# Kernel optimization log

Measured on AMD Instinct MI355X. Metric: run time of the kernel, lower is better.

Reference implementation:

```python
import jax, jax.numpy as jnp
import numpy as np

B, N, M, D, H = 4, 2048, 2048, 1024, 16
HD = D // H


def setup_inputs() -> dict:
    key = jax.random.key(0)
    ks = jax.random.split(key, 16)
    s = 1.0 / np.sqrt(D)
    inp = {
        "Q": jax.random.normal(ks[0], (B, N, D), jnp.float32),
        "K": jax.random.normal(ks[1], (B, M, D), jnp.float32),
        "V": jax.random.normal(ks[2], (B, M, D), jnp.float32),
        "attn_bias": jax.random.normal(ks[3], (B, N, M), jnp.float32),
        "mask": jax.random.randint(ks[4], (B, M), 0, 2).astype(bool),
        # linear params (torch nn.Linear: y = x @ W.T + b)
        "Wq": jax.random.uniform(ks[5], (D, D), jnp.float32, -s, s),
        "bq": jax.random.uniform(ks[6], (D,), jnp.float32, -s, s),
        "Wk": jax.random.uniform(ks[7], (D, D), jnp.float32, -s, s),
        "bk": jax.random.uniform(ks[8], (D,), jnp.float32, -s, s),
        "Wv": jax.random.uniform(ks[9], (D, D), jnp.float32, -s, s),
        "bv": jax.random.uniform(ks[10], (D,), jnp.float32, -s, s),
        "Wo": jax.random.uniform(ks[11], (D, D), jnp.float32, -s, s),
        "bo": jax.random.uniform(ks[12], (D,), jnp.float32, -s, s),
    }
    return inp


def reference(Q, K, V, attn_bias, mask, Wq, bq, Wk, bk, Wv, bv, Wo, bo):
    b, n, d = Q.shape
    m = K.shape[1]
    # bias (B,N,M) -> (B,1,N,M); mask (B,M) True = masked out (-inf)
    bias = attn_bias[:, None, :, :]
    bias = jnp.where(mask[:, None, None, :], -jnp.inf, bias)
    # projections, split heads: (B, H, len, head_dim)
    q = (Q @ Wq.T + bq).reshape(b, n, H, HD).transpose(0, 2, 1, 3)
    k = (K @ Wk.T + bk).reshape(b, m, H, HD).transpose(0, 2, 1, 3)
    v = (V @ Wv.T + bv).reshape(b, m, H, HD).transpose(0, 2, 1, 3)
    scale = 1.0 / np.sqrt(HD).astype(np.float32)
    attn = jnp.einsum("bhid,bhjd->bhij", q * scale, k) + bias
    attn = jax.nn.softmax(attn, axis=-1)
    out = jnp.einsum("bhij,bhjd->bhid", attn, v)
    out = out.transpose(0, 2, 1, 3).reshape(b, n, d)
    return out @ Wo.T + bo
```

## Files before the change

### kernel.cpp

```cpp
#include <hip/hip_runtime.h>
#include <hip/hip_bf16.h>

#define Bq 4
#define Nq 2048
#define Mq 2048
#define Dq 1024
#define Hq 16

typedef __attribute__((ext_vector_type(8))) short short8;
typedef __attribute__((ext_vector_type(4))) short short4v;
typedef __attribute__((ext_vector_type(4))) float floatx4;
typedef __attribute__((ext_vector_type(16))) float floatx16;
typedef __attribute__((ext_vector_type(4))) unsigned uint4v;

static __device__ __forceinline__ short f2bf(float f) {
    __hip_bfloat16 h = __float2bfloat16(f);
    short r;
    __builtin_memcpy(&r, &h, 2);
    return r;
}
static __device__ __forceinline__ float bf2f(short s) {
    unsigned u = ((unsigned)(unsigned short)s) << 16;
    float f;
    __builtin_memcpy(&f, &u, 4);
    return f;
}
static __device__ __forceinline__ unsigned cvtpk_bf16(float lo, float hi) {
    unsigned r;
    asm("v_cvt_pk_bf16_f32 %0, %1, %2" : "=v"(r) : "v"(lo), "v"(hi));
    return r;
}
static __device__ __forceinline__ void swap32(unsigned &a, unsigned &b) {
    asm("v_permlane32_swap_b32 %0, %1" : "+v"(a), "+v"(b));
}
static __device__ __forceinline__ float exp2_fast(float x) {
    float r;
    asm("v_exp_f32 %0, %1" : "=v"(r) : "v"(x));
    return r;
}
static __device__ __forceinline__ void gld16(const void* g, void* l) {
    __builtin_amdgcn_global_load_lds(
        (const __attribute__((address_space(1))) unsigned int*)g,
        (__attribute__((address_space(3))) unsigned int*)l, 16, 0, 0);
}

__global__ void bias_prep(const float* __restrict__ bias, const int* __restrict__ mask,
                          short* __restrict__ out)
{
    const long i = ((long)blockIdx.x * 256 + threadIdx.x) * 8;
    const int m = (int)(i & (Mq - 1));
    const int b = (int)(i >> 22);
    floatx4 f0 = *(const floatx4*)(bias + i);
    floatx4 f1 = *(const floatx4*)(bias + i + 4);
    const int* mp = mask + b * Mq + m;
    short8 o;
#pragma unroll
    for (int e = 0; e < 4; ++e) {
        o[e]     = mp[e]     ? f2bf(-1e38f) : f2bf(f0[e] * 1.44269504f);
        o[e + 4] = mp[e + 4] ? f2bf(-1e38f) : f2bf(f1[e] * 1.44269504f);
    }
    *(short8*)(out + i) = o;
}

__global__ void cvt_bf(const float* __restrict__ s0, const float* __restrict__ s1,
                       const float* __restrict__ s2, const float* __restrict__ s3,
                       short* __restrict__ out, long per)
{
    const int z = blockIdx.y;
    const float* s = (z == 0) ? s0 : (z == 1) ? s1 : (z == 2) ? s2 : s3;
    short* d = out + (long)z * per;
    const long i = ((long)blockIdx.x * 256 + threadIdx.x) * 8;
    floatx4 f0 = *(const floatx4*)(s + i);
    floatx4 f1 = *(const floatx4*)(s + i + 4);
    short8 o;
#pragma unroll
    for (int e = 0; e < 4; ++e) { o[e] = f2bf(f0[e]); o[e + 4] = f2bf(f1[e]); }
    *(short8*)(d + i) = o;
}

struct GB {
    const short* A[3];
    const short* W[3];
    const float* bias[3];
    void* C[3];
    float scale[3];
    int omode[3];
};

__global__ __launch_bounds__(256, 3)
void gemm_all(GB gb, int K)
{
    __shared__ __align__(16) short As[2][128 * 32];
    __shared__ __align__(16) short Bs[2][128 * 32];

    const int z = blockIdx.z;
    const short* Ap = gb.A[z];
    const short* Wp = gb.W[z];

    const int tid = threadIdx.x;
    const int lane = tid & 63;
    const int wid = tid >> 6;
    const int wr = wid >> 1, wc = wid & 1;
    const int g = lane >> 4, c = lane & 15;
    const long row0 = (long)blockIdx.x * 128;
    const int col0 = blockIdx.y * 128;

    const int R0 = tid >> 2;
    const int ub = (tid & 3) ^ ((R0 >> 1) & 3);
    const short* asrc = Ap + (row0 + R0) * (long)K + ub * 8;
    const short* bsrc = Wp + ((long)col0 + R0) * K + ub * 8;

    floatx4 acc[4][4];
#pragma unroll
    for (int i = 0; i < 4; ++i)
#pragma unroll
        for (int j = 0; j < 4; ++j) acc[i][j] = (floatx4)0.0f;

#define GSTAGE(buf, koff) do {                                                \
        char* ad = (char*)As + (buf) * 8192 + wid * 1024;                     \
        char* bd = (char*)Bs + (buf) * 8192 + wid * 1024;                     \
        gld16(asrc + (koff), ad);                                             \
        gld16(asrc + 64L * K + (koff), ad + 4096);                            \
        gld16(bsrc + (koff), bd);                                             \
        gld16(bsrc + 64L * K + (koff), bd + 4096);                            \
    } while (0)

    GSTAGE(0, 0);
    __syncthreads();

    int buf = 0;
    for (int kt = 0; kt < K; kt += 32) {
        if (kt + 32 < K) GSTAGE(buf ^ 1, kt + 32);
        short8* As8 = (short8*)((char*)As + buf * 8192);
        short8* Bs8 = (short8*)((char*)Bs + buf * 8192);
        short8 af[4], bfq[4];
#pragma unroll
        for (int fm = 0; fm < 4; ++fm) {
            const int r = wr * 64 + fm * 16 + c;
            af[fm] = As8[r * 4 + (g ^ ((r >> 1) & 3))];
        }
#pragma unroll
        for (int fn = 0; fn < 4; ++fn) {
            const int cc = wc * 64 + fn * 16 + c;
            bfq[fn] = Bs8[cc * 4 + (g ^ ((cc >> 1) & 3))];
        }
#pragma unroll
        for (int fm = 0; fm < 4; ++fm)
#pragma unroll
            for (int fn = 0; fn < 4; ++fn)
                acc[fm][fn] = __builtin_amdgcn_mfma_f32_16x16x32_bf16(af[fm], bfq[fn], acc[fm][fn], 0, 0, 0);
        __syncthreads();
        buf ^= 1;
    }
#undef GSTAGE

    const float sc = gb.scale[z];
    const float* bp = gb.bias[z];
    const int om = gb.omode[z];
    void* Cp = gb.C[z];
#pragma unroll
    for (int fn = 0; fn < 4; ++fn) {
        const int ccol = col0 + wc * 64 + fn * 16 + c;
        const float bv = bp[ccol];
#pragma unroll
        for (int fm = 0; fm < 4; ++fm) {
            const long r0 = row0 + wr * 64 + fm * 16 + g * 4;
#pragma unroll
            for (int reg = 0; reg < 4; ++reg) {
                const float val = (acc[fm][fn][reg] + bv) * sc;
                const long rr = r0 + reg;
                if (om == 0) {
                    ((short*)Cp)[rr * Dq + ccol] = f2bf(val);
                } else if (om == 1) {
                    const long idx = ((long)(rr >> 11) * Dq + ccol) * (long)Mq + (rr & (Mq - 1));
                    ((short*)Cp)[idx] = f2bf(val);
                } else {
                    ((float*)Cp)[rr * Dq + ccol] = val;
                }
            }
        }
    }
}

__global__ __launch_bounds__(256, 4)
void attn_fused(const short* __restrict__ qg_, const short* __restrict__ kg_,
                const short* __restrict__ vtg, const short* __restrict__ bmg,
                short* __restrict__ outg)
{
    __shared__ __align__(16) short k_lds[2][64 * 64];
    __shared__ __align__(16) short v_lds[2][64 * 64];

    const int tid = threadIdx.x;
    const int lane = tid & 63;
    const int w = tid >> 6;
    const int hi = lane >> 5;
    const int q31 = lane & 31;

    const int blk = blockIdx.x;
    const int bh = blk & 63;
    const int qt = blk >> 6;
    const int b = bh >> 4, h = bh & 15;

    const long qbase = (long)b * Nq + qt * 128 + w * 32;

    short8 qf[4];
#pragma unroll
    for (int ks = 0; ks < 4; ++ks)
        qf[ks] = *(const short8*)(qg_ + (qbase + q31) * Dq + h * 64 + ks * 16 + hi * 8);

    floatx16 oa[2];
    oa[0] = (floatx16)0.0f; oa[1] = (floatx16)0.0f;
    float m_s = -1e37f, l_s = 0.0f;

    const int sr = tid >> 3;
    const int su = (tid & 7) ^ (sr & 7);
    const char* ksrc = (const char*)(kg_ + ((long)b * Mq + sr) * Dq + h * 64 + su * 8);
    const char* vsrc = (const char*)(vtg + ((long)b * Dq + h * 64 + sr) * Mq + su * 8);

#define STAGE(bf, kt2) do {                                                   \
        const long j0b = (long)(kt2) * 64;                                    \
        char* kd = (char*)k_lds + (bf) * 8192 + w * 1024;                     \
        char* vd = (char*)v_lds + (bf) * 8192 + w * 1024;                     \
        gld16(ksrc + j0b * (Dq * 2), kd);                                     \
        gld16(ksrc + (j0b + 32) * (Dq * 2), kd + 4096);                       \
        gld16(vsrc + j0b * 2, vd);                                            \
        gld16(vsrc + 32L * Mq * 2 + j0b * 2, vd + 4096);                      \
    } while (0)

    STAGE(0, 0);
    __syncthreads();

    int buf = 0;
    for (int kt = 0; kt < 32; ++kt) {
        if (kt < 31) STAGE(buf ^ 1, kt + 1);
        const short* brow = bmg + (qbase + q31) * Mq + (long)kt * 64;
        short4v bb[8];
#pragma unroll
        for (int kg = 0; kg < 2; ++kg)
#pragma unroll
            for (int Qh = 0; Qh < 4; ++Qh)
                bb[kg * 4 + Qh] = *(const short4v*)(brow + kg * 32 + Qh * 8 + hi * 4);

        const char* kb = (const char*)k_lds + buf * 8192;
        const char* vb = (const char*)v_lds + buf * 8192;

        floatx16 sa[2];
#pragma unroll
        for (int kg = 0; kg < 2; ++kg)
#pragma unroll
            for (int Qh = 0; Qh < 4; ++Qh) {
                const short4v b4 = bb[kg * 4 + Qh];
#pragma unroll
                for (int e = 0; e < 4; ++e)
                    sa[kg][Qh * 4 + e] = bf2f(b4[e]);
            }
#pragma unroll
        for (int kg = 0; kg < 2; ++kg) {
            short8 kf[4];
#pragma unroll
            for (int ks = 0; ks < 4; ++ks) {
                const int r = kg * 32 + q31;
                const int up = (2 * ks + hi) ^ (r & 7);
                kf[ks] = *(const short8*)(kb + r * 128 + up * 16);
            }
#pragma unroll
            for (int ks = 0; ks < 4; ++ks)
                sa[kg] = __builtin_amdgcn_mfma_f32_32x32x16_bf16(kf[ks], qf[ks], sa[kg], 0, 0, 0);
        }

        float p[32];
#pragma unroll
        for (int kg = 0; kg < 2; ++kg)
#pragma unroll
            for (int j = 0; j < 16; ++j)
                p[kg * 16 + j] = sa[kg][j];
        float t16[16];
#pragma unroll
        for (int i = 0; i < 16; ++i) t16[i] = fmaxf(p[2 * i], p[2 * i + 1]);
#pragma unroll
        for (int i = 0; i < 8; ++i) t16[i] = fmaxf(t16[2 * i], t16[2 * i + 1]);
        t16[0] = fmaxf(fmaxf(fmaxf(t16[0], t16[1]), fmaxf(t16[2], t16[3])),
                       fmaxf(fmaxf(t16[4], t16[5]), fmaxf(t16[6], t16[7])));
        const float pm = fmaxf(t16[0], __shfl_xor(t16[0], 32));
        if (!__all(pm <= m_s + 11.5f)) {
            const float mn = fmaxf(m_s, pm);
            const float al = exp2_fast(m_s - mn);
            l_s *= al;
            oa[0] *= al; oa[1] *= al;
            m_s = mn;
        }
#pragma unroll
        for (int i = 0; i < 32; ++i) p[i] = exp2_fast(p[i] - m_s);
        float s16[16];
#pragma unroll
        for (int i = 0; i < 16; ++i) s16[i] = p[2 * i] + p[2 * i + 1];
#pragma unroll
        for (int i = 0; i < 8; ++i) s16[i] = s16[2 * i] + s16[2 * i + 1];
        float rs = ((s16[0] + s16[1]) + (s16[2] + s16[3])) +
                   ((s16[4] + s16[5]) + (s16[6] + s16[7]));
        rs += __shfl_xor(rs, 32);
        l_s += rs;

        uint4v pw[4];
#pragma unroll
        for (int kg = 0; kg < 2; ++kg) {
            unsigned w0 = cvtpk_bf16(p[kg * 16 + 0], p[kg * 16 + 1]);
            unsigned w1 = cvtpk_bf16(p[kg * 16 + 2], p[kg * 16 + 3]);
            unsigned w2 = cvtpk_bf16(p[kg * 16 + 4], p[kg * 16 + 5]);
            unsigned w3 = cvtpk_bf16(p[kg * 16 + 6], p[kg * 16 + 7]);
            swap32(w0, w2); swap32(w1, w3);
            pw[kg * 2][0] = w0; pw[kg * 2][1] = w1; pw[kg * 2][2] = w2; pw[kg * 2][3] = w3;
            unsigned w4 = cvtpk_bf16(p[kg * 16 + 8],  p[kg * 16 + 9]);
            unsigned w5 = cvtpk_bf16(p[kg * 16 + 10], p[kg * 16 + 11]);
            unsigned w6 = cvtpk_bf16(p[kg * 16 + 12], p[kg * 16 + 13]);
            unsigned w7 = cvtpk_bf16(p[kg * 16 + 14], p[kg * 16 + 15]);
            swap32(w4, w6); swap32(w5, w7);
            pw[kg * 2 + 1][0] = w4; pw[kg * 2 + 1][1] = w5; pw[kg * 2 + 1][2] = w6; pw[kg * 2 + 1][3] = w7;
        }

#pragma unroll
        for (int dg = 0; dg < 2; ++dg) {
            short8 vf[4];
#pragma unroll
            for (int ks = 0; ks < 4; ++ks) {
                const int r = dg * 32 + q31;
                const int up = (2 * ks + hi) ^ (r & 7);
                vf[ks] = *(const short8*)(vb + r * 128 + up * 16);
            }
#pragma unroll
            for (int ks = 0; ks < 4; ++ks)
                oa[dg] = __builtin_amdgcn_mfma_f32_32x32x16_bf16(
                    vf[ks], __builtin_bit_cast(short8, pw[ks]), oa[dg], 0, 0, 0);
        }
        __syncthreads();
        buf ^= 1;
    }
#undef STAGE

    const float invl = 1.0f / l_s;
    short* op = outg + (qbase + q31) * Dq + h * 64;
#pragma unroll
    for (int dg = 0; dg < 2; ++dg)
#pragma unroll
        for (int Qh = 0; Qh < 4; ++Qh) {
            short4v t;
#pragma unroll
            for (int e = 0; e < 4; ++e)
                t[e] = f2bf(oa[dg][Qh * 4 + e] * invl);
            *(short4v*)(op + dg * 32 + Qh * 8 + hi * 4) = t;
        }
}

extern "C" void kernel_launch(void* const* d_in, const int* in_sizes, int n_in,
                              void* d_out, int out_size, void* d_ws, size_t ws_size,
                              hipStream_t stream)
{
    const float* Q    = (const float*)d_in[0];
    const float* K    = (const float*)d_in[1];
    const float* V    = (const float*)d_in[2];
    const float* bias = (const float*)d_in[3];
    const int*   mask = (const int*)d_in[4];
    const float* Wq   = (const float*)d_in[5];
    const float* bq   = (const float*)d_in[6];
    const float* Wk   = (const float*)d_in[7];
    const float* bk   = (const float*)d_in[8];
    const float* Wv   = (const float*)d_in[9];
    const float* bv   = (const float*)d_in[10];
    const float* Wo   = (const float*)d_in[11];
    const float* bo   = (const float*)d_in[12];

    const size_t TSZ = (size_t)Bq * Nq * Dq;
    short* q_ws  = (short*)d_ws;
    short* k_ws  = q_ws  + TSZ;
    short* vt_ws = k_ws  + TSZ;
    short* a_ws  = vt_ws + TSZ;
    short* bm_ws = a_ws  + TSZ;
    short* w_ws  = bm_ws + 2 * TSZ;
    short* qin_ws = a_ws;
    short* kin_ws = bm_ws;
    short* vin_ws = bm_ws + TSZ;
    (void)ws_size;

    cvt_bf<<<dim3(512, 4), dim3(256), 0, stream>>>(Wq, Wk, Wv, Wo, w_ws, (long)Dq * Dq);
    cvt_bf<<<dim3(4096, 3), dim3(256), 0, stream>>>(Q, K, V, V, qin_ws, (long)TSZ);

    GB g1{};
    g1.A[0] = qin_ws; g1.A[1] = kin_ws; g1.A[2] = vin_ws;
    g1.W[0] = w_ws; g1.W[1] = w_ws + Dq * Dq; g1.W[2] = w_ws + 2 * Dq * Dq;
    g1.bias[0] = bq; g1.bias[1] = bk; g1.bias[2] = bv;
    g1.C[0] = q_ws; g1.C[1] = k_ws; g1.C[2] = vt_ws;
    g1.scale[0] = 0.125f * 1.44269504f; g1.scale[1] = 1.0f; g1.scale[2] = 1.0f;
    g1.omode[0] = 0; g1.omode[1] = 0; g1.omode[2] = 1;
    gemm_all<<<dim3(64, 8, 3), dim3(256), 0, stream>>>(g1, Dq);

    bias_prep<<<dim3(8192), dim3(256), 0, stream>>>(bias, mask, bm_ws);

    attn_fused<<<dim3(1024), dim3(256), 0, stream>>>(q_ws, k_ws, vt_ws, bm_ws, a_ws);

    GB g2{};
    g2.A[0] = a_ws;
    g2.W[0] = w_ws + 3 * Dq * Dq;
    g2.bias[0] = bo;
    g2.C[0] = d_out;
    g2.scale[0] = 1.0f;
    g2.omode[0] = 2;
    gemm_all<<<dim3(64, 8, 1), dim3(256), 0, stream>>>(g2, Dq);
}
```

Measured before the change: 328.3 us.

## Unroll attention loop by two with prefetched bias registers and MFMA priority

Restructures the flash-attention main loop into a two-step unrolled body with fixed LDS buffer pointers. The bias tile for the next key block is prefetched into a second register set, so global bias loads overlap the current block's compute instead of sitting on its critical path. MFMA sections are wrapped in s_setprio to raise wave priority during matrix work, and accumulators are split into scalar vectors to help register allocation. The second bias register set raises VGPR pressure, which could lower occupancy.

```diff
diff --git a/kernel.cpp b/kernel.cpp
--- a/kernel.cpp
+++ b/kernel.cpp
@@ -208,14 +208,14 @@
     for (int ks = 0; ks < 4; ++ks)
         qf[ks] = *(const short8*)(qg_ + (qbase + q31) * Dq + h * 64 + ks * 16 + hi * 8);
 
-    floatx16 oa[2];
-    oa[0] = (floatx16)0.0f; oa[1] = (floatx16)0.0f;
+    floatx16 oa0 = (floatx16)0.0f, oa1 = (floatx16)0.0f;
     float m_s = -1e37f, l_s = 0.0f;
 
     const int sr = tid >> 3;
     const int su = (tid & 7) ^ (sr & 7);
     const char* ksrc = (const char*)(kg_ + ((long)b * Mq + sr) * Dq + h * 64 + su * 8);
     const char* vsrc = (const char*)(vtg + ((long)b * Dq + h * 64 + sr) * Mq + su * 8);
+    const short* bbase = bmg + (qbase + q31) * Mq + hi * 4;
 
 #define STAGE(bf, kt2) do {                                                   \
         const long j0b = (long)(kt2) * 64;                                    \
@@ -227,128 +227,180 @@
         gld16(vsrc + 32L * Mq * 2 + j0b * 2, vd + 4096);                      \
     } while (0)
 
+#define LOADBB(bb, kt2) do {                                                  \
+        const short* brow_ = bbase + (long)(kt2) * 64;                        \
+        _Pragma("unroll")                                                     \
+        for (int kg = 0; kg < 2; ++kg)                                        \
+            _Pragma("unroll")                                                 \
+            for (int Qh = 0; Qh < 4; ++Qh)                                    \
+                bb[kg * 4 + Qh] = *(const short4v*)(brow_ + kg * 32 + Qh * 8);\
+    } while (0)
+
+#define COMPUTE(kb, vb, bb) do {                                              \
+        floatx16 sa0, sa1;                                                    \
+        _Pragma("unroll")                                                     \
+        for (int Qh = 0; Qh < 4; ++Qh)                                        \
+            _Pragma("unroll")                                                 \
+            for (int e = 0; e < 4; ++e) {                                     \
+                sa0[Qh * 4 + e] = bf2f(bb[Qh][e]);                            \
+                sa1[Qh * 4 + e] = bf2f(bb[4 + Qh][e]);                        \
+            }                                                                 \
+        {                                                                     \
+            short8 kf[4];                                                     \
+            _Pragma("unroll")                                                 \
+            for (int ks = 0; ks < 4; ++ks)                                    \
+                kf[ks] = *(const short8*)((kb) + q31 * 128 + (((2 * ks + hi) ^ (q31 & 7)) * 16)); \
+            __builtin_amdgcn_s_setprio(1);                                    \
+            _Pragma("unroll")                                                 \
+            for (int ks = 0; ks < 4; ++ks)                                    \
+                sa0 = __builtin_amdgcn_mfma_f32_32x32x16_bf16(kf[ks], qf[ks], sa0, 0, 0, 0); \
+            __builtin_amdgcn_s_setprio(0);                                    \
+        }                                                                     \
+        {                                                                     \
+            short8 kf[4];                                                     \
+            const int r1 = 32 + q31;                                          \
+            _Pragma("unroll")                                                 \
+            for (int ks = 0; ks < 4; ++ks)                                    \
+                kf[ks] = *(const short8*)((kb) + r1 * 128 + (((2 * ks + hi) ^ (r1 & 7)) * 16)); \
+            __builtin_amdgcn_s_setprio(1);                                    \
+            _Pragma("unroll")                                                 \
+            for (int ks = 0; ks < 4; ++ks)                                    \
+                sa1 = __builtin_amdgcn_mfma_f32_32x32x16_bf16(kf[ks], qf[ks], sa1, 0, 0, 0); \
+            __builtin_amdgcn_s_setprio(0);                                    \
+        }                                                                     \
+                                 \
+        {                                                                     \
+            float a0 = fmaxf(fmaxf(sa0[0], sa0[1]), fmaxf(sa0[2], sa0[3]));   \
+            float a1 = fmaxf(fmaxf(sa0[4], sa0[5]), fmaxf(sa0[6], sa0[7]));   \
+            float a2 = fmaxf(fmaxf(sa0[8], sa0[9]), fmaxf(sa0[10], sa0[11])); \
+            float a3 = fmaxf(fmaxf(sa0[12], sa0[13]), fmaxf(sa0[14], sa0[15]));\
+            float a4 = fmaxf(fmaxf(sa1[0], sa1[1]), fmaxf(sa1[2], sa1[3]));   \
+            float a5 = fmaxf(fmaxf(sa1[4], sa1[5]), fmaxf(sa1[6], sa1[7]));   \
+            float a6 = fmaxf(fmaxf(sa1[8], sa1[9]), fmaxf(sa1[10], sa1[11])); \
+            float a7 = fmaxf(fmaxf(sa1[12], sa1[13]), fmaxf(sa1[14], sa1[15]));\
+            float pm = fmaxf(fmaxf(fmaxf(a0, a1), fmaxf(a2, a3)),             \
+                             fmaxf(fmaxf(a4, a5), fmaxf(a6, a7)));            \
+            pm = fmaxf(pm, __shfl_xor(pm, 32));                               \
+            if (!__all(pm <= m_s + 11.5f)) {                                  \
+                const float mn = fmaxf(m_s, pm);                              \
+                const float al = exp2_fast(m_s - mn);                         \
+                l_s *= al;                                                    \
+                oa0 *= al; oa1 *= al;                                         \
+                m_s = mn;                                                     \
+            }                                                                 \
+        }                                                                     \
+        _Pragma("unroll")                                                     \
+        for (int j = 0; j < 16; ++j) {                                        \
+            sa0[j] = exp2_fast(sa0[j] - m_s);                                 \
+            sa1[j] = exp2_fast(sa1[j] - m_s);                                 \
+        }                                                                     \
+        {                                                                     \
+            const float t0 = (sa0[0] + sa0[1]) + (sa0[2] + sa0[3]);           \
+            const float t1 = (sa0[4] + sa0[5]) + (sa0[6] + sa0[7]);           \
+            const float t2 = (sa0[8] + sa0[9]) + (sa0[10] + sa0[11]);         \
+            const float t3 = (sa0[12] + sa0[13]) + (sa0[14] + sa0[15]);       \
+            const float t4 = (sa1[0] + sa1[1]) + (sa1[2] + sa1[3]);           \
+            const float t5 = (sa1[4] + sa1[5]) + (sa1[6] + sa1[7]);           \
+            const float t6 = (sa1[8] + sa1[9]) + (sa1[10] + sa1[11]);         \
+            const float t7 = (sa1[12] + sa1[13]) + (sa1[14] + sa1[15]);       \
+            float rs = ((t0 + t1) + (t2 + t3)) + ((t4 + t5) + (t6 + t7));     \
+            rs += __shfl_xor(rs, 32);                                         \
+            l_s += rs;                                                        \
+        }                                                                     \
+        uint4v pw0, pw1, pw2, pw3;                                            \
+        {                                                                     \
+            unsigned w0 = cvtpk_bf16(sa0[0], sa0[1]);                         \
+            unsigned w1 = cvtpk_bf16(sa0[2], sa0[3]);                         \
+            unsigned w2 = cvtpk_bf16(sa0[4], sa0[5]);                         \
+            unsigned w3 = cvtpk_bf16(sa0[6], sa0[7]);                         \
+            swap32(w0, w2); swap32(w1, w3);                                   \
+            pw0[0] = w0; pw0[1] = w1; pw0[2] = w2; pw0[3] = w3;               \
+            unsigned w4 = cvtpk_bf16(sa0[8], sa0[9]);                         \
+            unsigned w5 = cvtpk_bf16(sa0[10], sa0[11]);                       \
+            unsigned w6 = cvtpk_bf16(sa0[12], sa0[13]);                       \
+            unsigned w7 = cvtpk_bf16(sa0[14], sa0[15]);                       \
+            swap32(w4, w6); swap32(w5, w7);                                   \
+            pw1[0] = w4; pw1[1] = w5; pw1[2] = w6; pw1[3] = w7;               \
+            unsigned x0 = cvtpk_bf16(sa1[0], sa1[1]);                         \
+            unsigned x1 = cvtpk_bf16(sa1[2], sa1[3]);                         \
+            unsigned x2 = cvtpk_bf16(sa1[4], sa1[5]);                         \
+            unsigned x3 = cvtpk_bf16(sa1[6], sa1[7]);                         \
+            swap32(x0, x2); swap32(x1, x3);                                   \
+            pw2[0] = x0; pw2[1] = x1; pw2[2] = x2; pw2[3] = x3;               \
+            unsigned x4 = cvtpk_bf16(sa1[8], sa1[9]);                         \
+            unsigned x5 = cvtpk_bf16(sa1[10], sa1[11]);                       \
+            unsigned x6 = cvtpk_bf16(sa1[12], sa1[13]);                       \
+            unsigned x7 = cvtpk_bf16(sa1[14], sa1[15]);                       \
+            swap32(x4, x6); swap32(x5, x7);                                   \
+            pw3[0] = x4; pw3[1] = x5; pw3[2] = x6; pw3[3] = x7;               \
+        }                                                                     \
+        {                                                                     \
+            short8 vf[4];                                                     \
+            _Pragma("unroll")                                                 \
+            for (int ks = 0; ks < 4; ++ks)                                    \
+                vf[ks] = *(const short8*)((vb) + q31 * 128 + (((2 * ks + hi) ^ (q31 & 7)) * 16)); \
+            __builtin_amdgcn_s_setprio(1);                                    \
+            oa0 = __builtin_amdgcn_mfma_f32_32x32x16_bf16(vf[0], __builtin_bit_cast(short8, pw0), oa0, 0, 0, 0); \
+            oa0 = __builtin_amdgcn_mfma_f32_32x32x16_bf16(vf[1], __builtin_bit_cast(short8, pw1), oa0, 0, 0, 0); \
+            oa0 = __builtin_amdgcn_mfma_f32_32x32x16_bf16(vf[2], __builtin_bit_cast(short8, pw2), oa0, 0, 0, 0); \
+            oa0 = __builtin_amdgcn_mfma_f32_32x32x16_bf16(vf[3], __builtin_bit_cast(short8, pw3), oa0, 0, 0, 0); \
+            __builtin_amdgcn_s_setprio(0);                                    \
+        }                                                                     \
+        {                                                                     \
+            short8 vf[4];                                                     \
+            const int r1 = 32 + q31;                                          \
+            _Pragma("unroll")                                                 \
+            for (int ks = 0; ks < 4; ++ks)                                    \
+                vf[ks] = *(const short8*)((vb) + r1 * 128 + (((2 * ks + hi) ^ (r1 & 7)) * 16)); \
+            __builtin_amdgcn_s_setprio(1);                                    \
+            oa1 = __builtin_amdgcn_mfma_f32_32x32x16_bf16(vf[0], __builtin_bit_cast(short8, pw0), oa1, 0, 0, 0); \
+            oa1 = __builtin_amdgcn_mfma_f32_32x32x16_bf16(vf[1], __builtin_bit_cast(short8, pw1), oa1, 0, 0, 0); \
+            oa1 = __builtin_amdgcn_mfma_f32_32x32x16_bf16(vf[2], __builtin_bit_cast(short8, pw2), oa1, 0, 0, 0); \
+            oa1 = __builtin_amdgcn_mfma_f32_32x32x16_bf16(vf[3], __builtin_bit_cast(short8, pw3), oa1, 0, 0, 0); \
+            __builtin_amdgcn_s_setprio(0);                                    \
+        }                                                                     \
+    } while (0)
+
+    short4v bbA[8], bbB[8];
+    const char* kb0 = (const char*)k_lds;
+    const char* kb1 = (const char*)k_lds + 8192;
+    const char* vb0 = (const char*)v_lds;
+    const char* vb1 = (const char*)v_lds + 8192;
+
     STAGE(0, 0);
+    LOADBB(bbA, 0);
     __syncthreads();
 
-    int buf = 0;
-    for (int kt = 0; kt < 32; ++kt) {
-        if (kt < 31) STAGE(buf ^ 1, kt + 1);
-        const short* brow = bmg + (qbase + q31) * Mq + (long)kt * 64;
-        short4v bb[8];
-#pragma unroll
-        for (int kg = 0; kg < 2; ++kg)
-#pragma unroll
-            for (int Qh = 0; Qh < 4; ++Qh)
-                bb[kg * 4 + Qh] = *(const short4v*)(brow + kg * 32 + Qh * 8 + hi * 4);
-
-        const char* kb = (const char*)k_lds + buf * 8192;
-        const char* vb = (const char*)v_lds + buf * 8192;
-
-        floatx16 sa[2];
-#pragma unroll
-        for (int kg = 0; kg < 2; ++kg)
-#pragma unroll
-            for (int Qh = 0; Qh < 4; ++Qh) {
-                const short4v b4 = bb[kg * 4 + Qh];
-#pragma unroll
-                for (int e = 0; e < 4; ++e)
-                    sa[kg][Qh * 4 + e] = bf2f(b4[e]);
-            }
-#pragma unroll
-        for (int kg = 0; kg < 2; ++kg) {
-            short8 kf[4];
-#pragma unroll
-            for (int ks = 0; ks < 4; ++ks) {
-                const int r = kg * 32 + q31;
-                const int up = (2 * ks + hi) ^ (r & 7);
-                kf[ks] = *(const short8*)(kb + r * 128 + up * 16);
-            }
-#pragma unroll
-            for (int ks = 0; ks < 4; ++ks)
-                sa[kg] = __builtin_amdgcn_mfma_f32_32x32x16_bf16(kf[ks], qf[ks], sa[kg], 0, 0, 0);
+    for (int it = 0; it < 16; ++it) {
+        const int t0 = 2 * it;
+        STAGE(1, t0 + 1);
+        LOADBB(bbB, t0 + 1);
+        COMPUTE(kb0, vb0, bbA);
+        __syncthreads();
+        if (it < 15) {
+            STAGE(0, t0 + 2);
+            LOADBB(bbA, t0 + 2);
         }
-
-        float p[32];
-#pragma unroll
-        for (int kg = 0; kg < 2; ++kg)
-#pragma unroll
-            for (int j = 0; j < 16; ++j)
-                p[kg * 16 + j] = sa[kg][j];
-        float t16[16];
-#pragma unroll
-        for (int i = 0; i < 16; ++i) t16[i] = fmaxf(p[2 * i], p[2 * i + 1]);
-#pragma unroll
-        for (int i = 0; i < 8; ++i) t16[i] = fmaxf(t16[2 * i], t16[2 * i + 1]);
-        t16[0] = fmaxf(fmaxf(fmaxf(t16[0], t16[1]), fmaxf(t16[2], t16[3])),
-                       fmaxf(fmaxf(t16[4], t16[5]), fmaxf(t16[6], t16[7])));
-        const float pm = fmaxf(t16[0], __shfl_xor(t16[0], 32));
-        if (!__all(pm <= m_s + 11.5f)) {
-            const float mn = fmaxf(m_s, pm);
-            const float al = exp2_fast(m_s - mn);
-            l_s *= al;
-            oa[0] *= al; oa[1] *= al;
-            m_s = mn;
-        }
-#pragma unroll
-        for (int i = 0; i < 32; ++i) p[i] = exp2_fast(p[i] - m_s);
-        float s16[16];
-#pragma unroll
-        for (int i = 0; i < 16; ++i) s16[i] = p[2 * i] + p[2 * i + 1];
-#pragma unroll
-        for (int i = 0; i < 8; ++i) s16[i] = s16[2 * i] + s16[2 * i + 1];
-        float rs = ((s16[0] + s16[1]) + (s16[2] + s16[3])) +
-                   ((s16[4] + s16[5]) + (s16[6] + s16[7]));
-        rs += __shfl_xor(rs, 32);
-        l_s += rs;
-
-        uint4v pw[4];
-#pragma unroll
-        for (int kg = 0; kg < 2; ++kg) {
-            unsigned w0 = cvtpk_bf16(p[kg * 16 + 0], p[kg * 16 + 1]);
-            unsigned w1 = cvtpk_bf16(p[kg * 16 + 2], p[kg * 16 + 3]);
-            unsigned w2 = cvtpk_bf16(p[kg * 16 + 4], p[kg * 16 + 5]);
-            unsigned w3 = cvtpk_bf16(p[kg * 16 + 6], p[kg * 16 + 7]);
-            swap32(w0, w2); swap32(w1, w3);
-            pw[kg * 2][0] = w0; pw[kg * 2][1] = w1; pw[kg * 2][2] = w2; pw[kg * 2][3] = w3;
-            unsigned w4 = cvtpk_bf16(p[kg * 16 + 8],  p[kg * 16 + 9]);
-            unsigned w5 = cvtpk_bf16(p[kg * 16 + 10], p[kg * 16 + 11]);
-            unsigned w6 = cvtpk_bf16(p[kg * 16 + 12], p[kg * 16 + 13]);
-            unsigned w7 = cvtpk_bf16(p[kg * 16 + 14], p[kg * 16 + 15]);
-            swap32(w4, w6); swap32(w5, w7);
-            pw[kg * 2 + 1][0] = w4; pw[kg * 2 + 1][1] = w5; pw[kg * 2 + 1][2] = w6; pw[kg * 2 + 1][3] = w7;
-        }
-
-#pragma unroll
-        for (int dg = 0; dg < 2; ++dg) {
-            short8 vf[4];
-#pragma unroll
-            for (int ks = 0; ks < 4; ++ks) {
-                const int r = dg * 32 + q31;
-                const int up = (2 * ks + hi) ^ (r & 7);
-                vf[ks] = *(const short8*)(vb + r * 128 + up * 16);
-            }
-#pragma unroll
-            for (int ks = 0; ks < 4; ++ks)
-                oa[dg] = __builtin_amdgcn_mfma_f32_32x32x16_bf16(
-                    vf[ks], __builtin_bit_cast(short8, pw[ks]), oa[dg], 0, 0, 0);
-        }
+        COMPUTE(kb1, vb1, bbB);
         __syncthreads();
-        buf ^= 1;
     }
 #undef STAGE
+#undef LOADBB
+#undef COMPUTE
 
     const float invl = 1.0f / l_s;
     short* op = outg + (qbase + q31) * Dq + h * 64;
 #pragma unroll
-    for (int dg = 0; dg < 2; ++dg)
-#pragma unroll
-        for (int Qh = 0; Qh < 4; ++Qh) {
-            short4v t;
-#pragma unroll
-            for (int e = 0; e < 4; ++e)
-                t[e] = f2bf(oa[dg][Qh * 4 + e] * invl);
-            *(short4v*)(op + dg * 32 + Qh * 8 + hi * 4) = t;
+    for (int Qh = 0; Qh < 4; ++Qh) {
+        short4v t0v, t1v;
+#pragma unroll
+        for (int e = 0; e < 4; ++e) {
+            t0v[e] = f2bf(oa0[Qh * 4 + e] * invl);
+            t1v[e] = f2bf(oa1[Qh * 4 + e] * invl);
         }
+        *(short4v*)(op + Qh * 8 + hi * 4) = t0v;
+        *(short4v*)(op + 32 + Qh * 8 + hi * 4) = t1v;
+    }
 }
 
 extern "C" void kernel_launch(void* const* d_in, const int* in_sizes, int n_in,
```

New measurement: 393.5 us. +19.8%, slower.
